# Kernel optimization log

Measured on AMD Instinct MI355X. Metric: run time of the kernel, lower is better.

The kernel has to match this reference:

```python
import jax, jax.numpy as jnp
import numpy as np

B, S, E, Q = 4, 4096, 1024, 8  # batch, seq, embed_dim, n_qubits


def setup_inputs() -> dict:
    key = jax.random.key(0)
    k1, k2, k3 = jax.random.split(key, 3)
    x = jax.random.normal(k1, (B, S, E), dtype=jnp.float32)
    W_enc = jax.random.normal(k2, (Q, E), dtype=jnp.float32) * (1.0 / np.sqrt(E))
    W_dec = jax.random.normal(k3, (E, Q), dtype=jnp.float32) * (1.0 / np.sqrt(Q))
    return {"x": x, "W_enc": W_enc, "W_dec": W_dec}


def reference(x, W_enc, W_dec):
    # encode tokens to rotation angles: [B,S,Q]
    angles = jnp.einsum('bse,qe->bsq', x, W_enc)
    c = jnp.cos(angles)
    # Analytic state-vector result of the circuit:
    #   RX(theta_i) on |0> then CNOT chain + ring closure, measure <Z_i>.
    # Heisenberg picture gives:
    #   <Z_0> = prod_{j=1..Q-1} cos(theta_j)
    #   <Z_i> = prod_{j=0..i}   cos(theta_j)   (i >= 1)
    p = jnp.cumprod(c, axis=-1)                      # prefix products
    q0 = jnp.prod(c[..., 1:], axis=-1, keepdims=True)
    q = jnp.concatenate([q0, p[..., 1:]], axis=-1)   # [B,S,Q] expvals
    # decode back to embed_dim and add residual
    return jnp.einsum('bsq,eq->bse', q, W_dec) + x
```

## Files before the change

kernel.cpp:

```cpp
#include <hip/hip_runtime.h>


typedef float v2f __attribute__((ext_vector_type(2)));
typedef float v4f __attribute__((ext_vector_type(4)));

#define EDIM 1024
#define QDIM 8
#define NTOK 16384
#define BLOCK 256
#define T 4
#define GRID (NTOK / T)

template<int CTRL>
__device__ __forceinline__ float dpp_add(float v) {
    int m = __builtin_amdgcn_update_dpp(0, __float_as_int(v), CTRL, 0xF, 0xF, true);
    return v + __int_as_float(m);
}

__device__ __forceinline__ float wave_sum63(float v) {
    v = dpp_add<0x111>(v);
    v = dpp_add<0x112>(v);
    v = dpp_add<0x114>(v);
    v = dpp_add<0x118>(v);
    v = dpp_add<0x142>(v);
    v = dpp_add<0x143>(v);
    return v;
}

__global__ __launch_bounds__(BLOCK, 2)
void qattn_kernel(const float* __restrict__ x,
                  const float* __restrict__ W_enc,
                  const float* __restrict__ W_dec,
                  float* __restrict__ out)
{
    __shared__ float red[T][4][QDIM];

    const int t    = threadIdx.x;
    const int lane = t & 63;
    const int wave = t >> 6;
    const int e0   = t * 4;

    const int tok0 = blockIdx.x * T;

    v4f xv[T];
#pragma unroll
    for (int i = 0; i < T; ++i)
        xv[i] = *(const v4f*)(x + (size_t)(tok0 + i) * EDIM + e0);

    v4f we[QDIM / 2][2];
#pragma unroll
    for (int q = 0; q < QDIM; ++q)
        *((v2f*)&we[q >> 1][0] + 0) = (v2f){0.f, 0.f};
    v4f wenc[QDIM];
#pragma unroll
    for (int q = 0; q < QDIM; ++q)
        wenc[q] = *(const v4f*)(W_enc + q * EDIM + e0);

    v4f wdlo[4], wdhi[4];
#pragma unroll
    for (int j = 0; j < 4; ++j) {
        wdlo[j] = *(const v4f*)(W_dec + (e0 + j) * QDIM);
        wdhi[j] = *(const v4f*)(W_dec + (e0 + j) * QDIM + 4);
    }

    float ang[T][QDIM];
#pragma unroll
    for (int i = 0; i < T; ++i) {
        v2f x01 = (v2f){xv[i].x, xv[i].y};
        v2f x23 = (v2f){xv[i].z, xv[i].w};
#pragma unroll
        for (int q = 0; q < QDIM; ++q) {
            v2f w01 = (v2f){wenc[q].x, wenc[q].y};
            v2f w23 = (v2f){wenc[q].z, wenc[q].w};
            v2f acc = x01 * w01;
            acc = __builtin_elementwise_fma(x23, w23, acc);
            ang[i][q] = acc.x + acc.y;
        }
    }

#pragma unroll
    for (int i = 0; i < T; ++i)
#pragma unroll
        for (int q = 0; q < QDIM; ++q)
            ang[i][q] = wave_sum63(ang[i][q]);

    if (lane == 63) {
#pragma unroll
        for (int i = 0; i < T; ++i) {
            *(v4f*)&red[i][wave][0] = (v4f){ang[i][0], ang[i][1], ang[i][2], ang[i][3]};
            *(v4f*)&red[i][wave][4] = (v4f){ang[i][4], ang[i][5], ang[i][6], ang[i][7]};
        }
    }
    __syncthreads();

#pragma unroll
    for (int i = 0; i < T; ++i) {
        v4f slo = (v4f){0.f, 0.f, 0.f, 0.f};
        v4f shi = (v4f){0.f, 0.f, 0.f, 0.f};
#pragma unroll
        for (int w = 0; w < 4; ++w) {
            slo += *(const v4f*)&red[i][w][0];
            shi += *(const v4f*)&red[i][w][4];
        }
        float c[QDIM];
        c[0] = __cosf(slo.x); c[1] = __cosf(slo.y);
        c[2] = __cosf(slo.z); c[3] = __cosf(slo.w);
        c[4] = __cosf(shi.x); c[5] = __cosf(shi.y);
        c[6] = __cosf(shi.z); c[7] = __cosf(shi.w);

        float qv[QDIM];
        float q0 = c[1];
#pragma unroll
        for (int q = 2; q < QDIM; ++q) q0 *= c[q];
        qv[0] = q0;
        float p = c[0];
#pragma unroll
        for (int q = 1; q < QDIM; ++q) { p *= c[q]; qv[q] = p; }

        v4f qlo = (v4f){qv[0], qv[1], qv[2], qv[3]};
        v4f qhi = (v4f){qv[4], qv[5], qv[6], qv[7]};

        float oacc[4];
#pragma unroll
        for (int j = 0; j < 4; ++j) {
            v4f a = qlo * wdlo[j];
            a = __builtin_elementwise_fma(qhi, wdhi[j], a);
            v2f h = (v2f){a.x, a.y} + (v2f){a.z, a.w};
            oacc[j] = h.x + h.y;
        }
        v4f o = xv[i] + (v4f){oacc[0], oacc[1], oacc[2], oacc[3]};
        __builtin_nontemporal_store(o, (v4f*)(out + (size_t)(tok0 + i) * EDIM + e0));
    }
}

extern "C" void kernel_launch(void* const* d_in, const int* in_sizes, int n_in,
                              void* d_out, int out_size, void* d_ws, size_t ws_size,
                              hipStream_t stream) {
    const float* x     = (const float*)d_in[0];
    const float* W_enc = (const float*)d_in[1];
    const float* W_dec = (const float*)d_in[2];
    float* out         = (float*)d_out;

    hipLaunchKernelGGL(qattn_kernel, dim3(GRID), dim3(BLOCK), 0, stream,
                       x, W_enc, W_dec, out);
}
```

Measured before the change: 33.76 us.

## Split fused kernel into angle-encode and decode kernels via workspace buffer

```diff
diff --git a/kernel.cpp b/kernel.cpp
--- a/kernel.cpp
+++ b/kernel.cpp
@@ -9,7 +9,9 @@
 #define NTOK 16384
 #define BLOCK 256
 #define T 4
-#define GRID (NTOK / T)
+#define GRID1 (NTOK / T)
+#define TK2 8
+#define GRID2 (NTOK / TK2)
 
 template<int CTRL>
 __device__ __forceinline__ float dpp_add(float v) {
@@ -28,10 +30,9 @@
 }
 
 __global__ __launch_bounds__(BLOCK, 2)
-void qattn_kernel(const float* __restrict__ x,
+void qattn_angles(const float* __restrict__ x,
                   const float* __restrict__ W_enc,
-                  const float* __restrict__ W_dec,
-                  float* __restrict__ out)
+                  float* __restrict__ qbuf)
 {
     __shared__ float red[T][4][QDIM];
 
@@ -39,7 +40,6 @@
     const int lane = t & 63;
     const int wave = t >> 6;
     const int e0   = t * 4;
-
     const int tok0 = blockIdx.x * T;
 
     v4f xv[T];
@@ -47,14 +47,77 @@
     for (int i = 0; i < T; ++i)
         xv[i] = *(const v4f*)(x + (size_t)(tok0 + i) * EDIM + e0);
 
-    v4f we[QDIM / 2][2];
-#pragma unroll
-    for (int q = 0; q < QDIM; ++q)
-        *((v2f*)&we[q >> 1][0] + 0) = (v2f){0.f, 0.f};
     v4f wenc[QDIM];
 #pragma unroll
     for (int q = 0; q < QDIM; ++q)
         wenc[q] = *(const v4f*)(W_enc + q * EDIM + e0);
+
+    float ang[T][QDIM];
+#pragma unroll
+    for (int i = 0; i < T; ++i) {
+        v2f x01 = (v2f){xv[i].x, xv[i].y};
+        v2f x23 = (v2f){xv[i].z, xv[i].w};
+#pragma unroll
+        for (int q = 0; q < QDIM; ++q) {
+            v2f acc = x01 * (v2f){wenc[q].x, wenc[q].y};
+            acc = __builtin_elementwise_fma(x23, (v2f){wenc[q].z, wenc[q].w}, acc);
+            ang[i][q] = acc.x + acc.y;
+        }
+    }
+
+#pragma unroll
+    for (int i = 0; i < T; ++i)
+#pragma unroll
+        for (int q = 0; q < QDIM; ++q)
+            ang[i][q] = wave_sum63(ang[i][q]);
+
+    if (lane == 63) {
+#pragma unroll
+        for (int i = 0; i < T; ++i) {
+            *(v4f*)&red[i][wave][0] = (v4f){ang[i][0], ang[i][1], ang[i][2], ang[i][3]};
+            *(v4f*)&red[i][wave][4] = (v4f){ang[i][4], ang[i][5], ang[i][6], ang[i][7]};
+        }
+    }
+    __syncthreads();
+
+    if (t < T) {
+        v4f slo = (v4f){0.f, 0.f, 0.f, 0.f};
+        v4f shi = (v4f){0.f, 0.f, 0.f, 0.f};
+#pragma unroll
+        for (int w = 0; w < 4; ++w) {
+            slo += *(const v4f*)&red[t][w][0];
+            shi += *(const v4f*)&red[t][w][4];
+        }
+        float c[QDIM];
+        c[0] = __cosf(slo.x); c[1] = __cosf(slo.y);
+        c[2] = __cosf(slo.z); c[3] = __cosf(slo.w);
+        c[4] = __cosf(shi.x); c[5] = __cosf(shi.y);
+        c[6] = __cosf(shi.z); c[7] = __cosf(shi.w);
+
+        float qv[QDIM];
+        float q0 = c[1];
+#pragma unroll
+        for (int q = 2; q < QDIM; ++q) q0 *= c[q];
+        qv[0] = q0;
+        float p = c[0];
+#pragma unroll
+        for (int q = 1; q < QDIM; ++q) { p *= c[q]; qv[q] = p; }
+
+        float* dst = qbuf + (size_t)(tok0 + t) * QDIM;
+        *(v4f*)(dst)     = (v4f){qv[0], qv[1], qv[2], qv[3]};
+        *(v4f*)(dst + 4) = (v4f){qv[4], qv[5], qv[6], qv[7]};
+    }
+}
+
+__global__ __launch_bounds__(BLOCK, 2)
+void qattn_decode(const float* __restrict__ x,
+                  const float* __restrict__ W_dec,
+                  const float* __restrict__ qbuf,
+                  float* __restrict__ out)
+{
+    const int t  = threadIdx.x;
+    const int e0 = t * 4;
+    const int tok0 = blockIdx.x * TK2;
 
     v4f wdlo[4], wdhi[4];
 #pragma unroll
@@ -63,6 +126,57 @@
         wdhi[j] = *(const v4f*)(W_dec + (e0 + j) * QDIM + 4);
     }
 
+#pragma unroll
+    for (int i = 0; i < TK2; ++i) {
+        const size_t tok = (size_t)(tok0 + i);
+        v4f qlo = *(const v4f*)(qbuf + tok * QDIM);
+        v4f qhi = *(const v4f*)(qbuf + tok * QDIM + 4);
+        v4f xv  = *(const v4f*)(x + tok * EDIM + e0);
+
+        float oacc[4];
+#pragma unroll
+        for (int j = 0; j < 4; ++j) {
+            v4f a = qlo * wdlo[j];
+            a = __builtin_elementwise_fma(qhi, wdhi[j], a);
+            v2f h = (v2f){a.x, a.y} + (v2f){a.z, a.w};
+            oacc[j] = h.x + h.y;
+        }
+        v4f o = xv + (v4f){oacc[0], oacc[1], oacc[2], oacc[3]};
+        __builtin_nontemporal_store(o, (v4f*)(out + tok * EDIM + e0));
+    }
+}
+
+__global__ __launch_bounds__(BLOCK, 2)
+void qattn_fused(const float* __restrict__ x,
+                 const float* __restrict__ W_enc,
+                 const float* __restrict__ W_dec,
+                 float* __restrict__ out)
+{
+    __shared__ float red[T][4][QDIM];
+
+    const int t    = threadIdx.x;
+    const int lane = t & 63;
+    const int wave = t >> 6;
+    const int e0   = t * 4;
+    const int tok0 = blockIdx.x * T;
+
+    v4f xv[T];
+#pragma unroll
+    for (int i = 0; i < T; ++i)
+        xv[i] = *(const v4f*)(x + (size_t)(tok0 + i) * EDIM + e0);
+
+    v4f wenc[QDIM];
+#pragma unroll
+    for (int q = 0; q < QDIM; ++q)
+        wenc[q] = *(const v4f*)(W_enc + q * EDIM + e0);
+
+    v4f wdlo[4], wdhi[4];
+#pragma unroll
+    for (int j = 0; j < 4; ++j) {
+        wdlo[j] = *(const v4f*)(W_dec + (e0 + j) * QDIM);
+        wdhi[j] = *(const v4f*)(W_dec + (e0 + j) * QDIM + 4);
+    }
+
     float ang[T][QDIM];
 #pragma unroll
     for (int i = 0; i < T; ++i) {
@@ -70,10 +184,8 @@
         v2f x23 = (v2f){xv[i].z, xv[i].w};
 #pragma unroll
         for (int q = 0; q < QDIM; ++q) {
-            v2f w01 = (v2f){wenc[q].x, wenc[q].y};
-            v2f w23 = (v2f){wenc[q].z, wenc[q].w};
-            v2f acc = x01 * w01;
-            acc = __builtin_elementwise_fma(x23, w23, acc);
+            v2f acc = x01 * (v2f){wenc[q].x, wenc[q].y};
+            acc = __builtin_elementwise_fma(x23, (v2f){wenc[q].z, wenc[q].w}, acc);
             ang[i][q] = acc.x + acc.y;
         }
     }
@@ -141,6 +253,15 @@
     const float* W_dec = (const float*)d_in[2];
     float* out         = (float*)d_out;
 
-    hipLaunchKernelGGL(qattn_kernel, dim3(GRID), dim3(BLOCK), 0, stream,
-                       x, W_enc, W_dec, out);
-}
+    const size_t need = (size_t)NTOK * QDIM * sizeof(float);
+    if (ws_size >= need) {
+        float* qbuf = (float*)d_ws;
+        hipLaunchKernelGGL(qattn_angles, dim3(GRID1), dim3(BLOCK), 0, stream,
+                           x, W_enc, qbuf);
+        hipLaunchKernelGGL(qattn_decode, dim3(GRID2), dim3(BLOCK), 0, stream,
+                           x, W_dec, qbuf, out);
+    } else {
+        hipLaunchKernelGGL(qattn_fused, dim3(GRID1), dim3(BLOCK), 0, stream,
+                           x, W_enc, W_dec, out);
+    }
+}
```

Result: slower. 41.57 us (+23.1%).

## Double tokens per block and compute cos/prefix products once in wave 0

Applied to the files above, without the earlier changes.

```diff
diff --git a/kernel.cpp b/kernel.cpp
--- a/kernel.cpp
+++ b/kernel.cpp
@@ -8,7 +8,7 @@
 #define QDIM 8
 #define NTOK 16384
 #define BLOCK 256
-#define T 4
+#define T 8
 #define GRID (NTOK / T)
 
 template<int CTRL>
@@ -27,6 +27,13 @@
     return v;
 }
 
+template<int K>
+__device__ __forceinline__ float scan_mul_step(float p, int laneq) {
+    int m = __builtin_amdgcn_update_dpp(0, __float_as_int(p), 0x110 | K, 0xF, 0xF, true);
+    float tmul = (laneq >= K) ? __int_as_float(m) : 1.0f;
+    return p * tmul;
+}
+
 __global__ __launch_bounds__(BLOCK, 2)
 void qattn_kernel(const float* __restrict__ x,
                   const float* __restrict__ W_enc,
@@ -34,12 +41,12 @@
                   float* __restrict__ out)
 {
     __shared__ float red[T][4][QDIM];
+    __shared__ float qv_s[T][QDIM];
 
     const int t    = threadIdx.x;
     const int lane = t & 63;
     const int wave = t >> 6;
     const int e0   = t * 4;
-
     const int tok0 = blockIdx.x * T;
 
     v4f xv[T];
@@ -47,14 +54,64 @@
     for (int i = 0; i < T; ++i)
         xv[i] = *(const v4f*)(x + (size_t)(tok0 + i) * EDIM + e0);
 
-    v4f we[QDIM / 2][2];
-#pragma unroll
-    for (int q = 0; q < QDIM; ++q)
-        *((v2f*)&we[q >> 1][0] + 0) = (v2f){0.f, 0.f};
     v4f wenc[QDIM];
 #pragma unroll
     for (int q = 0; q < QDIM; ++q)
         wenc[q] = *(const v4f*)(W_enc + q * EDIM + e0);
+
+#pragma unroll
+    for (int h = 0; h < 2; ++h) {
+        float ang[4][QDIM];
+#pragma unroll
+        for (int i = 0; i < 4; ++i) {
+            const int ii = h * 4 + i;
+            v2f x01 = (v2f){xv[ii].x, xv[ii].y};
+            v2f x23 = (v2f){xv[ii].z, xv[ii].w};
+#pragma unroll
+            for (int q = 0; q < QDIM; ++q) {
+                v2f acc = x01 * (v2f){wenc[q].x, wenc[q].y};
+                acc = __builtin_elementwise_fma(x23, (v2f){wenc[q].z, wenc[q].w}, acc);
+                ang[i][q] = acc.x + acc.y;
+            }
+        }
+#pragma unroll
+        for (int i = 0; i < 4; ++i)
+#pragma unroll
+            for (int q = 0; q < QDIM; ++q)
+                ang[i][q] = wave_sum63(ang[i][q]);
+
+        if (lane == 63) {
+#pragma unroll
+            for (int i = 0; i < 4; ++i) {
+                *(v4f*)&red[h * 4 + i][wave][0] =
+                    (v4f){ang[i][0], ang[i][1], ang[i][2], ang[i][3]};
+                *(v4f*)&red[h * 4 + i][wave][4] =
+                    (v4f){ang[i][4], ang[i][5], ang[i][6], ang[i][7]};
+            }
+        }
+    }
+    __syncthreads();
+
+    if (wave == 0) {
+        const int tk = lane >> 3;
+        const int q  = lane & 7;
+        float s = red[tk][0][q] + red[tk][1][q] + red[tk][2][q] + red[tk][3][q];
+        float c = __cosf(s);
+
+        float p = c;
+        p = scan_mul_step<1>(p, q);
+        p = scan_mul_step<2>(p, q);
+        p = scan_mul_step<4>(p, q);
+
+        float b = (q == 0) ? 1.0f : c;
+        b = scan_mul_step<1>(b, q);
+        b = scan_mul_step<2>(b, q);
+        b = scan_mul_step<4>(b, q);
+
+        if (q > 0)  qv_s[tk][q] = p;
+        if (q == 7) qv_s[tk][0] = b;
+    }
+    __syncthreads();
 
     v4f wdlo[4], wdhi[4];
 #pragma unroll
@@ -62,71 +119,17 @@
         wdlo[j] = *(const v4f*)(W_dec + (e0 + j) * QDIM);
         wdhi[j] = *(const v4f*)(W_dec + (e0 + j) * QDIM + 4);
     }
-
-    float ang[T][QDIM];
 #pragma unroll
     for (int i = 0; i < T; ++i) {
-        v2f x01 = (v2f){xv[i].x, xv[i].y};
-        v2f x23 = (v2f){xv[i].z, xv[i].w};
-#pragma unroll
-        for (int q = 0; q < QDIM; ++q) {
-            v2f w01 = (v2f){wenc[q].x, wenc[q].y};
-            v2f w23 = (v2f){wenc[q].z, wenc[q].w};
-            v2f acc = x01 * w01;
-            acc = __builtin_elementwise_fma(x23, w23, acc);
-            ang[i][q] = acc.x + acc.y;
-        }
-    }
-
-#pragma unroll
-    for (int i = 0; i < T; ++i)
-#pragma unroll
-        for (int q = 0; q < QDIM; ++q)
-            ang[i][q] = wave_sum63(ang[i][q]);
-
-    if (lane == 63) {
-#pragma unroll
-        for (int i = 0; i < T; ++i) {
-            *(v4f*)&red[i][wave][0] = (v4f){ang[i][0], ang[i][1], ang[i][2], ang[i][3]};
-            *(v4f*)&red[i][wave][4] = (v4f){ang[i][4], ang[i][5], ang[i][6], ang[i][7]};
-        }
-    }
-    __syncthreads();
-
-#pragma unroll
-    for (int i = 0; i < T; ++i) {
-        v4f slo = (v4f){0.f, 0.f, 0.f, 0.f};
-        v4f shi = (v4f){0.f, 0.f, 0.f, 0.f};
-#pragma unroll
-        for (int w = 0; w < 4; ++w) {
-            slo += *(const v4f*)&red[i][w][0];
-            shi += *(const v4f*)&red[i][w][4];
-        }
-        float c[QDIM];
-        c[0] = __cosf(slo.x); c[1] = __cosf(slo.y);
-        c[2] = __cosf(slo.z); c[3] = __cosf(slo.w);
-        c[4] = __cosf(shi.x); c[5] = __cosf(shi.y);
-        c[6] = __cosf(shi.z); c[7] = __cosf(shi.w);
-
-        float qv[QDIM];
-        float q0 = c[1];
-#pragma unroll
-        for (int q = 2; q < QDIM; ++q) q0 *= c[q];
-        qv[0] = q0;
-        float p = c[0];
-#pragma unroll
-        for (int q = 1; q < QDIM; ++q) { p *= c[q]; qv[q] = p; }
-
-        v4f qlo = (v4f){qv[0], qv[1], qv[2], qv[3]};
-        v4f qhi = (v4f){qv[4], qv[5], qv[6], qv[7]};
-
+        v4f qlo = *(const v4f*)&qv_s[i][0];
+        v4f qhi = *(const v4f*)&qv_s[i][4];
         float oacc[4];
 #pragma unroll
         for (int j = 0; j < 4; ++j) {
             v4f a = qlo * wdlo[j];
             a = __builtin_elementwise_fma(qhi, wdhi[j], a);
-            v2f h = (v2f){a.x, a.y} + (v2f){a.z, a.w};
-            oacc[j] = h.x + h.y;
+            v2f hh = (v2f){a.x, a.y} + (v2f){a.z, a.w};
+            oacc[j] = hh.x + hh.y;
         }
         v4f o = xv[i] + (v4f){oacc[0], oacc[1], oacc[2], oacc[3]};
         __builtin_nontemporal_store(o, (v4f*)(out + (size_t)(tok0 + i) * EDIM + e0));
```

New measurement: 30.67 us. 1.1x faster.
